# Kernel tuning notes

Measured on AMD Instinct MI355X. Metric: run time of the kernel, lower is better.

The kernel has to match this reference:

```python
import jax, jax.numpy as jnp
import numpy as np

VOCAB, EMBED = 50000, 256
MODULES, HEADS, HID = 2, 4, 64
B, S = 8, 2048
LABELS = 16


def setup_inputs() -> dict:
    key = jax.random.key(0)
    ks = jax.random.split(key, 12)
    seqs = jax.random.randint(ks[0], (B, S), 0, VOCAB)
    emb = jax.random.normal(ks[1], (VOCAB, EMBED), jnp.float32) * 0.02
    Wq = jax.random.normal(ks[2], (MODULES, HEADS, HID, EMBED), jnp.float32) * (1.0 / np.sqrt(EMBED))
    bq = jax.random.normal(ks[3], (MODULES, HEADS, HID), jnp.float32) * 0.01
    Wk = jax.random.normal(ks[4], (MODULES, HEADS, HID, EMBED), jnp.float32) * (1.0 / np.sqrt(EMBED))
    bk = jax.random.normal(ks[5], (MODULES, HEADS, HID), jnp.float32) * 0.01
    Wv = jax.random.normal(ks[6], (MODULES, HEADS, HID, EMBED), jnp.float32) * (1.0 / np.sqrt(EMBED))
    bv = jax.random.normal(ks[7], (MODULES, HEADS, HID), jnp.float32) * 0.01
    Wz = jax.random.normal(ks[8], (MODULES, EMBED, HEADS * HID), jnp.float32) * (1.0 / np.sqrt(HEADS * HID))
    bz = jax.random.normal(ks[9], (MODULES, EMBED), jnp.float32) * 0.01
    Wo = jax.random.normal(ks[10], (LABELS, S * EMBED), jnp.float32) * (1.0 / np.sqrt(S * EMBED))
    bo = jax.random.normal(ks[11], (LABELS,), jnp.float32) * 0.01
    return {"seqs": seqs, "emb": emb, "Wq": Wq, "bq": bq, "Wk": Wk, "bk": bk,
            "Wv": Wv, "bv": bv, "Wz": Wz, "bz": bz, "Wo": Wo, "bo": bo}


def _forward(seqs, emb, Wq, bq, Wk, bk, Wv, bv, Wz, bz, Wo, bo):
    x = emb[seqs]  # [B, S, E]
    scale = jnp.float32(EMBED) ** 0.5
    for m in range(MODULES):
        # per-head projections with relu (dropout=0 / eval mode)
        Q = jax.nn.relu(jnp.einsum('bse,hde->bhsd', x, Wq[m]) + bq[m][None, :, None, :])
        K = jax.nn.relu(jnp.einsum('bse,hde->bhsd', x, Wk[m]) + bk[m][None, :, None, :])
        V = jax.nn.relu(jnp.einsum('bse,hde->bhsd', x, Wv[m]) + bv[m][None, :, None, :])
        QK = jnp.einsum('bhsd,bhtd->bhst', Q, K) / scale  # [B,H,S,S]
        # double softmax: first over the query axis (torch dim=1 of [B,S,S]),
        # then over the key axis (torch dim=2)
        A = jax.nn.softmax(QK, axis=2)
        A = jax.nn.softmax(A, axis=3)
        Z = jnp.einsum('bhst,bhtd->bhsd', A, V)  # [B,H,S,HID]
        Zall = jnp.transpose(Z, (0, 2, 1, 3)).reshape(x.shape[0], S, HEADS * HID)
        ZF = jnp.einsum('bsk,ek->bse', Zall, Wz[m]) + bz[m]
        x = ZF + x  # residual (layer_norm=False)
    Xf = x.reshape(x.shape[0], S * EMBED)
    y = jax.nn.sigmoid(Xf @ Wo.T + bo)
    return y


def reference(seqs, emb, Wq, bq, Wk, bk, Wv, bv, Wz, bz, Wo, bo):
    return _forward(seqs, emb, Wq, bq, Wk, bk, Wv, bv, Wz, bz, Wo, bo)
```

## Files before the change

### kernel.cpp

```cpp
#include <hip/hip_runtime.h>
#include <math.h>

#define Bb 8
#define Ss 2048
#define Ee 256
#define Hh 4
#define Dd 64

typedef unsigned short u16;
typedef unsigned int u32;
typedef __attribute__((ext_vector_type(8))) short bf16x8;
typedef __attribute__((ext_vector_type(4))) float f32x4;

__device__ __forceinline__ u16 f2bf(float f) {
  union { float f; u32 u; } c; c.f = f;
  return (u16)((c.u + 0x7FFFu + ((c.u >> 16) & 1u)) >> 16);
}
__device__ __forceinline__ float bf2f(u16 u) {
  union { u32 u; float f; } c; c.u = ((u32)u) << 16;
  return c.f;
}
__device__ __forceinline__ float bf2fs(short s) { return bf2f((u16)s); }

__global__ __launch_bounds__(256) void k_w2b(const float* __restrict__ src,
                                             u16* __restrict__ dst) {
  int idx = (blockIdx.x * 256 + threadIdx.x) * 4;
  float4 v = *reinterpret_cast<const float4*>(src + idx);
  ushort4 o;
  o.x = f2bf(v.x); o.y = f2bf(v.y); o.z = f2bf(v.z); o.w = f2bf(v.w);
  *reinterpret_cast<ushort4*>(dst + idx) = o;
}

__global__ __launch_bounds__(256) void k_gather(const int* __restrict__ seqs,
                                                const float* __restrict__ emb,
                                                float* __restrict__ x,
                                                u16* __restrict__ xb) {
  int idx = blockIdx.x * 256 + threadIdx.x;
  int row = idx >> 6, c4 = idx & 63;
  int tok = seqs[row];
  float4 v = reinterpret_cast<const float4*>(emb)[(size_t)tok * 64 + c4];
  reinterpret_cast<float4*>(x)[(size_t)row * 64 + c4] = v;
  ushort4 o;
  o.x = f2bf(v.x); o.y = f2bf(v.y); o.z = f2bf(v.z); o.w = f2bf(v.w);
  reinterpret_cast<ushort4*>(xb)[(size_t)row * 64 + c4] = o;
}

__global__ __launch_bounds__(256) void k_qkvm(const u16* __restrict__ xb,
    const u16* __restrict__ Wqb, const u16* __restrict__ Wkb, const u16* __restrict__ Wvb,
    const float* __restrict__ bq, const float* __restrict__ bk, const float* __restrict__ bv,
    u16* __restrict__ Qf, u16* __restrict__ Kf, u16* __restrict__ Vf, int mod) {
  __shared__ short Xs[128][72];
  __shared__ short Ws[128][72];
  int tid = threadIdx.x;
  int bn = blockIdx.x;
  int arr = bn >> 1, coff = (bn & 1) << 7;
  const u16* W = (arr == 0 ? Wqb : arr == 1 ? Wkb : Wvb) + (size_t)mod * 256 * 256;
  const float* bias = (arr == 0 ? bq : arr == 1 ? bk : bv) + mod * 256;
  u16* Out = (arr == 0 ? Qf : arr == 1 ? Kf : Vf);
  int s0 = blockIdx.y * 128;
  int lr = tid >> 1, lc = (tid & 1) << 5;
  int w = tid >> 6, lane = tid & 63, ml = lane & 15, q = lane >> 4;
  int sh = (w >> 1) << 6, th = (w & 1) << 6;
  f32x4 acc[4][4] = {};
  for (int k0 = 0; k0 < 256; k0 += 64) {
#pragma unroll
    for (int hh = 0; hh < 4; hh++) {
      *reinterpret_cast<bf16x8*>(&Xs[lr][lc + hh * 8]) =
          *reinterpret_cast<const bf16x8*>(xb + (size_t)(s0 + lr) * Ee + k0 + lc + hh * 8);
      *reinterpret_cast<bf16x8*>(&Ws[lr][lc + hh * 8]) =
          *reinterpret_cast<const bf16x8*>(W + (size_t)(coff + lr) * Ee + k0 + lc + hh * 8);
    }
    __syncthreads();
#pragma unroll
    for (int ks = 0; ks < 2; ks++) {
      bf16x8 af[4], bfr[4];
#pragma unroll
      for (int mt = 0; mt < 4; mt++)
        af[mt] = *reinterpret_cast<const bf16x8*>(&Xs[sh + mt * 16 + ml][ks * 32 + q * 8]);
#pragma unroll
      for (int nt = 0; nt < 4; nt++)
        bfr[nt] = *reinterpret_cast<const bf16x8*>(&Ws[th + nt * 16 + ml][ks * 32 + q * 8]);
#pragma unroll
      for (int mt = 0; mt < 4; mt++)
#pragma unroll
        for (int nt = 0; nt < 4; nt++)
          acc[mt][nt] = __builtin_amdgcn_mfma_f32_16x16x32_bf16(af[mt], bfr[nt], acc[mt][nt], 0, 0, 0);
    }
    __syncthreads();
  }
#pragma unroll
  for (int mt = 0; mt < 4; mt++)
#pragma unroll
    for (int nt = 0; nt < 4; nt++)
#pragma unroll
      for (int r = 0; r < 4; r++) {
        int gm = s0 + sh + mt * 16 + q * 4 + r;
        int cc = coff + th + nt * 16 + ml;
        float v = acc[mt][nt][r] + bias[cc];
        Out[(size_t)gm * Ee + cc] = f2bf(v > 0.f ? v : 0.f);
      }
}

__global__ __launch_bounds__(256) void k_vt(const u16* __restrict__ Vf,
                                            u16* __restrict__ Vt) {
  __shared__ u16 T[64][72];
  int tid = threadIdx.x;
  int t0 = blockIdx.x * 64;
  int z = blockIdx.y;
  int b = z >> 2, h = z & 3;
  int lr = tid >> 2, lc = (tid & 3) << 4;
#pragma unroll
  for (int hh = 0; hh < 2; hh++) {
    bf16x8 v = *reinterpret_cast<const bf16x8*>(
        Vf + (size_t)(b * Ss + t0 + lr) * Ee + h * Dd + lc + hh * 8);
#pragma unroll
    for (int j = 0; j < 8; j++) T[lr][lc + hh * 8 + j] = (u16)v[j];
  }
  __syncthreads();
#pragma unroll
  for (int j = 0; j < 16; j++) {
    Vt[((size_t)z * Dd + lr) * Ss + t0 + lc + j] = T[lc + j][lr];
  }
}

__global__ __launch_bounds__(256) void k_vsum(const u16* __restrict__ Vt,
                                              float* __restrict__ SV) {
  int z = blockIdx.y;
  int d = blockIdx.x * 4 + (threadIdx.x >> 6);
  int lane = threadIdx.x & 63;
  const u16* row = Vt + ((size_t)z * Dd + d) * Ss;
  float s = 0.f;
#pragma unroll
  for (int it = 0; it < 4; it++) {
    bf16x8 v = *reinterpret_cast<const bf16x8*>(row + it * 512 + lane * 8);
#pragma unroll
    for (int j = 0; j < 8; j++) s += bf2fs(v[j]);
  }
#pragma unroll
  for (int off = 32; off; off >>= 1) s += __shfl_xor(s, off);
  if (lane == 0) SV[(size_t)z * Dd + d] = s;
}

__global__ __launch_bounds__(256) void k_csum(const u16* __restrict__ Qf,
    const u16* __restrict__ Kf, float* __restrict__ icl) {
  __shared__ short Qs[128 * 72];
  __shared__ short Ks[128 * 72];
  __shared__ float csm[4][64];
  int tid = threadIdx.x;
  int z = blockIdx.y, b = z >> 2, h = z & 3;
  const u16* Qb = Qf + (size_t)b * Ss * Ee + h * Dd;
  const u16* Kb = Kf + (size_t)b * Ss * Ee + h * Dd;
  int t0 = blockIdx.x * 128;
  int lr = tid >> 1, lc = (tid & 1) << 5;
#pragma unroll
  for (int hh = 0; hh < 4; hh++)
    *reinterpret_cast<bf16x8*>(&Ks[lr * 72 + lc + hh * 8]) =
        *reinterpret_cast<const bf16x8*>(Kb + (size_t)(t0 + lr) * Ee + lc + hh * 8);
  int w = tid >> 6, lane = tid & 63, ml = lane & 15, q = lane >> 4;
  int sh = (w >> 1) << 6, th = (w & 1) << 6;
  float csum[4] = {};
  for (int s0 = 0; s0 < Ss; s0 += 128) {
    __syncthreads();
#pragma unroll
    for (int hh = 0; hh < 4; hh++)
      *reinterpret_cast<bf16x8*>(&Qs[lr * 72 + lc + hh * 8]) =
          *reinterpret_cast<const bf16x8*>(Qb + (size_t)(s0 + lr) * Ee + lc + hh * 8);
    __syncthreads();
    f32x4 acc[4][4] = {};
#pragma unroll
    for (int ks = 0; ks < 2; ks++) {
      bf16x8 af[4], bf[4];
#pragma unroll
      for (int mt = 0; mt < 4; mt++)
        af[mt] = *reinterpret_cast<const bf16x8*>(&Qs[(sh + mt * 16 + ml) * 72 + ks * 32 + q * 8]);
#pragma unroll
      for (int nt = 0; nt < 4; nt++)
        bf[nt] = *reinterpret_cast<const bf16x8*>(&Ks[(th + nt * 16 + ml) * 72 + ks * 32 + q * 8]);
#pragma unroll
      for (int mt = 0; mt < 4; mt++)
#pragma unroll
        for (int nt = 0; nt < 4; nt++)
          acc[mt][nt] = __builtin_amdgcn_mfma_f32_16x16x32_bf16(af[mt], bf[nt], acc[mt][nt], 0, 0, 0);
    }
#pragma unroll
    for (int nt = 0; nt < 4; nt++)
#pragma unroll
      for (int mt = 0; mt < 4; mt++)
#pragma unroll
        for (int r = 0; r < 4; r++)
          csum[nt] += __expf(acc[mt][nt][r] * 0.0625f);
  }
#pragma unroll
  for (int nt = 0; nt < 4; nt++) {
    csum[nt] += __shfl_xor(csum[nt], 16);
    csum[nt] += __shfl_xor(csum[nt], 32);
  }
  if (lane < 16) {
#pragma unroll
    for (int nt = 0; nt < 4; nt++) csm[w][nt * 16 + ml] = csum[nt];
  }
  __syncthreads();
  if (tid < 128) {
    int half = tid >> 6, c = tid & 63;
    float l = csm[half][c] + csm[half + 2][c];
    icl[(size_t)z * Ss + t0 + half * 64 + c] = 1.f / l;
  }
}

__global__ __launch_bounds__(256) void k_att(const u16* __restrict__ Qf,
    const u16* __restrict__ Kf, const u16* __restrict__ Vt,
    const float* __restrict__ icl, const float* __restrict__ SV,
    u16* __restrict__ Zb) {
  __shared__ short Qs[128 * 72];
  __shared__ short Ks[64 * 72];
  __shared__ short Vs[64 * 72];
  __shared__ short A2s[128 * 76];
  __shared__ float rs_s[2][128];
  int tid = threadIdx.x;
  int z = blockIdx.y, b = z >> 2, h = z & 3;
  const u16* Qb = Qf + (size_t)b * Ss * Ee + h * Dd;
  const u16* Kb = Kf + (size_t)b * Ss * Ee + h * Dd;
  const u16* VtZ = Vt + (size_t)z * Dd * Ss;
  const float* iclz = icl + (size_t)z * Ss;
  int s0 = blockIdx.x * 128;
  int lr = tid >> 1, lc = (tid & 1) << 5;
#pragma unroll
  for (int hh = 0; hh < 4; hh++)
    *reinterpret_cast<bf16x8*>(&Qs[lr * 72 + lc + hh * 8]) =
        *reinterpret_cast<const bf16x8*>(Qb + (size_t)(s0 + lr) * Ee + lc + hh * 8);
  int w = tid >> 6, lane = tid & 63, ml = lane & 15, q = lane >> 4;
  int ws = (w >> 1) << 6, wt = (w & 1) << 5;
  f32x4 acc2[2][4] = {};
  f32x4 rsv[4] = {};
  for (int t0 = 0; t0 < Ss; t0 += 64) {
    __syncthreads();
    if (tid < 128) {
      int r2 = tid >> 1, h2 = (tid & 1) << 5;
#pragma unroll
      for (int j = 0; j < 4; j++)
        *reinterpret_cast<bf16x8*>(&Ks[r2 * 72 + h2 + j * 8]) =
            *reinterpret_cast<const bf16x8*>(Kb + (size_t)(t0 + r2) * Ee + h2 + j * 8);
    } else {
      int t2 = tid - 128;
      int r2 = t2 >> 1, h2 = (t2 & 1) << 5;
#pragma unroll
      for (int j = 0; j < 4; j++)
        *reinterpret_cast<bf16x8*>(&Vs[r2 * 72 + h2 + j * 8]) =
            *reinterpret_cast<const bf16x8*>(VtZ + (size_t)r2 * Ss + t0 + h2 + j * 8);
    }
    __syncthreads();
    f32x4 acc[4][2] = {};
#pragma unroll
    for (int ks = 0; ks < 2; ks++) {
      bf16x8 af[4], bf[2];
#pragma unroll
      for (int mt = 0; mt < 4; mt++)
        af[mt] = *reinterpret_cast<const bf16x8*>(&Qs[(ws + mt * 16 + ml) * 72 + ks * 32 + q * 8]);
#pragma unroll
      for (int nt = 0; nt < 2; nt++)
        bf[nt] = *reinterpret_cast<const bf16x8*>(&Ks[(wt + nt * 16 + ml) * 72 + ks * 32 + q * 8]);
#pragma unroll
      for (int mt = 0; mt < 4; mt++)
#pragma unroll
        for (int nt = 0; nt < 2; nt++)
          acc[mt][nt] = __builtin_amdgcn_mfma_f32_16x16x32_bf16(af[mt], bf[nt], acc[mt][nt], 0, 0, 0);
    }
#pragma unroll
    for (int nt = 0; nt < 2; nt++) {
      float ic = iclz[t0 + wt + nt * 16 + ml];
#pragma unroll
      for (int mt = 0; mt < 4; mt++)
#pragma unroll
        for (int r = 0; r < 4; r++) {
          float e1 = __expf(acc[mt][nt][r] * 0.0625f) * ic;
          float p = e1 * (1.f + e1 * (0.5f + e1 * (0.166666667f +
                    e1 * (0.0416666667f + e1 * 0.00833333333f))));
          rsv[mt][r] += p;
          A2s[(ws + mt * 16 + q * 4 + r) * 76 + wt + nt * 16 + ml] = (short)f2bf(p);
        }
    }
    __syncthreads();
#pragma unroll
    for (int ks = 0; ks < 2; ks++) {
      bf16x8 af2[2], bv[4];
#pragma unroll
      for (int mt2 = 0; mt2 < 2; mt2++)
        af2[mt2] = *reinterpret_cast<const bf16x8*>(&A2s[(w * 32 + mt2 * 16 + ml) * 76 + ks * 32 + q * 8]);
#pragma unroll
      for (int nt = 0; nt < 4; nt++)
        bv[nt] = *reinterpret_cast<const bf16x8*>(&Vs[(nt * 16 + ml) * 72 + ks * 32 + q * 8]);
#pragma unroll
      for (int mt2 = 0; mt2 < 2; mt2++)
#pragma unroll
        for (int nt = 0; nt < 4; nt++)
          acc2[mt2][nt] = __builtin_amdgcn_mfma_f32_16x16x32_bf16(af2[mt2], bv[nt], acc2[mt2][nt], 0, 0, 0);
    }
  }
#pragma unroll
  for (int mt = 0; mt < 4; mt++)
#pragma unroll
    for (int r = 0; r < 4; r++) {
      float v = rsv[mt][r];
      v += __shfl_xor(v, 1); v += __shfl_xor(v, 2);
      v += __shfl_xor(v, 4); v += __shfl_xor(v, 8);
      if (ml == 0) rs_s[w & 1][ws + mt * 16 + q * 4 + r] = v;
    }
  __syncthreads();
  const float* SVz = SV + (size_t)z * Dd;
#pragma unroll
  for (int mt2 = 0; mt2 < 2; mt2++)
#pragma unroll
    for (int r = 0; r < 4; r++) {
      int row = w * 32 + mt2 * 16 + q * 4 + r;
      float inv = 1.f / (2048.f + rs_s[0][row] + rs_s[1][row]);
#pragma unroll
      for (int nt = 0; nt < 4; nt++) {
        float o = (SVz[nt * 16 + ml] + acc2[mt2][nt][r]) * inv;
        Zb[(size_t)(b * Ss + s0 + row) * Ee + h * Dd + nt * 16 + ml] = f2bf(o);
      }
    }
}

__global__ __launch_bounds__(256) void k_zfm(const u16* __restrict__ Zb,
    const u16* __restrict__ Wzb, const float* __restrict__ bzp,
    float* __restrict__ x, u16* __restrict__ xb, int mod) {
  __shared__ short Zs[128][72];
  __shared__ short Ws[128][72];
  int tid = threadIdx.x;
  int coff = blockIdx.x << 7;
  const u16* W = Wzb + (size_t)mod * 256 * 256;
  const float* bias = bzp + mod * Ee;
  int s0 = blockIdx.y * 128;
  int lr = tid >> 1, lc = (tid & 1) << 5;
  int w = tid >> 6, lane = tid & 63, ml = lane & 15, q = lane >> 4;
  int sh = (w >> 1) << 6, th = (w & 1) << 6;
  f32x4 acc[4][4] = {};
  for (int k0 = 0; k0 < 256; k0 += 64) {
#pragma unroll
    for (int hh = 0; hh < 4; hh++) {
      *reinterpret_cast<bf16x8*>(&Zs[lr][lc + hh * 8]) =
          *reinterpret_cast<const bf16x8*>(Zb + (size_t)(s0 + lr) * Ee + k0 + lc + hh * 8);
      *reinterpret_cast<bf16x8*>(&Ws[lr][lc + hh * 8]) =
          *reinterpret_cast<const bf16x8*>(W + (size_t)(coff + lr) * Ee + k0 + lc + hh * 8);
    }
    __syncthreads();
#pragma unroll
    for (int ks = 0; ks < 2; ks++) {
      bf16x8 af[4], bfr[4];
#pragma unroll
      for (int mt = 0; mt < 4; mt++)
        af[mt] = *reinterpret_cast<const bf16x8*>(&Zs[sh + mt * 16 + ml][ks * 32 + q * 8]);
#pragma unroll
      for (int nt = 0; nt < 4; nt++)
        bfr[nt] = *reinterpret_cast<const bf16x8*>(&Ws[th + nt * 16 + ml][ks * 32 + q * 8]);
#pragma unroll
      for (int mt = 0; mt < 4; mt++)
#pragma unroll
        for (int nt = 0; nt < 4; nt++)
          acc[mt][nt] = __builtin_amdgcn_mfma_f32_16x16x32_bf16(af[mt], bfr[nt], acc[mt][nt], 0, 0, 0);
    }
    __syncthreads();
  }
#pragma unroll
  for (int mt = 0; mt < 4; mt++)
#pragma unroll
    for (int nt = 0; nt < 4; nt++)
#pragma unroll
      for (int r = 0; r < 4; r++) {
        int gm = s0 + sh + mt * 16 + q * 4 + r;
        int gn = coff + th + nt * 16 + ml;
        float xv = x[(size_t)gm * Ee + gn] + acc[mt][nt][r] + bias[gn];
        x[(size_t)gm * Ee + gn] = xv;
        xb[(size_t)gm * Ee + gn] = f2bf(xv);
      }
}

__global__ __launch_bounds__(256) void k_final1(const float* __restrict__ x,
    const float* __restrict__ Wo, float* __restrict__ part) {
  int c = blockIdx.x, l = blockIdx.y, b = blockIdx.z;
  int tid = threadIdx.x;
  const float4* xr = reinterpret_cast<const float4*>(x + (size_t)b * (Ss * Ee) + c * 8192);
  const float4* wr = reinterpret_cast<const float4*>(Wo + (size_t)l * (Ss * Ee) + c * 8192);
  float sum = 0.f;
  for (int i = tid; i < 2048; i += 256) {
    float4 a = xr[i], w = wr[i];
    sum += a.x * w.x + a.y * w.y + a.z * w.z + a.w * w.w;
  }
  __shared__ float red[256];
  red[tid] = sum;
  __syncthreads();
  for (int o = 128; o; o >>= 1) {
    if (tid < o) red[tid] += red[tid + o];
    __syncthreads();
  }
  if (tid == 0) part[((b * 16 + l) << 6) + c] = red[0];
}

__global__ void k_final2(const float* __restrict__ part, const float* __restrict__ bo,
                         float* __restrict__ out) {
  int idx = threadIdx.x;
  int b = idx >> 4, l = idx & 15;
  float s = 0.f;
  for (int c = 0; c < 64; c++) s += part[((b * 16 + l) << 6) + c];
  s += bo[l];
  out[idx] = 1.f / (1.f + __expf(-s));
}

extern "C" void kernel_launch(void* const* d_in, const int* in_sizes, int n_in,
                              void* d_out, int out_size, void* d_ws, size_t ws_size,
                              hipStream_t stream) {
  const int*   seqs = (const int*)d_in[0];
  const float* emb  = (const float*)d_in[1];
  const float* Wq   = (const float*)d_in[2];
  const float* bq   = (const float*)d_in[3];
  const float* Wk   = (const float*)d_in[4];
  const float* bk   = (const float*)d_in[5];
  const float* Wv   = (const float*)d_in[6];
  const float* bv   = (const float*)d_in[7];
  const float* Wz   = (const float*)d_in[8];
  const float* bz   = (const float*)d_in[9];
  const float* Wo   = (const float*)d_in[10];
  const float* bo   = (const float*)d_in[11];
  float* out = (float*)d_out;
  float* ws  = (float*)d_ws;

  float* x    = ws;
  u16*   xb   = (u16*)(ws + 4194304);
  u16*   Qf   = (u16*)(ws + 6291456);
  u16*   Kf   = (u16*)(ws + 8388608);
  u16*   Vf   = (u16*)(ws + 10485760);
  u16*   Vt   = (u16*)(ws + 12582912);
  u16*   Zb   = (u16*)(ws + 14680064);
  float* SV   = ws + 16777216;
  float* part = ws + 16779264;
  u16*   Wqb  = (u16*)(ws + 16787456);
  u16*   Wkb  = (u16*)(ws + 16852992);
  u16*   Wvb  = (u16*)(ws + 16918528);
  u16*   Wzb  = (u16*)(ws + 16984064);
  float* icl  = ws + 17049600;

  k_gather<<<(Bb * Ss * 64) / 256, 256, 0, stream>>>(seqs, emb, x, xb);
  k_w2b<<<131072 / 1024, 256, 0, stream>>>(Wq, Wqb);
  k_w2b<<<131072 / 1024, 256, 0, stream>>>(Wk, Wkb);
  k_w2b<<<131072 / 1024, 256, 0, stream>>>(Wv, Wvb);
  k_w2b<<<131072 / 1024, 256, 0, stream>>>(Wz, Wzb);

  for (int m = 0; m < 2; m++) {
    k_qkvm<<<dim3(6, 128), 256, 0, stream>>>(xb, Wqb, Wkb, Wvb, bq, bk, bv, Qf, Kf, Vf, m);
    k_vt<<<dim3(32, 32), 256, 0, stream>>>(Vf, Vt);
    k_vsum<<<dim3(16, 32), 256, 0, stream>>>(Vt, SV);
    k_csum<<<dim3(16, 32), 256, 0, stream>>>(Qf, Kf, icl);
    k_att<<<dim3(16, 32), 256, 0, stream>>>(Qf, Kf, Vt, icl, SV, Zb);
    k_zfm<<<dim3(2, 128), 256, 0, stream>>>(Zb, Wzb, bz, x, xb, m);
  }

  k_final1<<<dim3(64, 16, 8), 256, 0, stream>>>(x, Wo, part);
  k_final2<<<1, 128, 0, stream>>>(part, bo, out);
}
```

Measured before the change: 539.1 us.

## Fold softmax scale into Q, hold K/Q fragments in registers, double-buffer Q tiles

Scales Q by 1/16 when it is stored so the attention kernels skip the per-element multiply. The column-sum kernel now outputs a negative log normalizer, so the attention kernel computes one exp(x+c) instead of an exp followed by a multiply. The K fragments in k_csum and the Q fragments in k_att are loaded once into registers instead of being staged in LDS, and k_csum double-buffers the Q tile to drop a barrier. The exp-series polynomial loses its last term and bf16 rounding is simplified to round-half-up, which changes numerics slightly and raises register pressure.

```diff
diff --git a/kernel.cpp b/kernel.cpp
--- a/kernel.cpp
+++ b/kernel.cpp
@@ -57,6 +57,7 @@
   const u16* W = (arr == 0 ? Wqb : arr == 1 ? Wkb : Wvb) + (size_t)mod * 256 * 256;
   const float* bias = (arr == 0 ? bq : arr == 1 ? bk : bv) + mod * 256;
   u16* Out = (arr == 0 ? Qf : arr == 1 ? Kf : Vf);
+  float oscale = (arr == 0) ? 0.0625f : 1.0f;
   int s0 = blockIdx.y * 128;
   int lr = tid >> 1, lc = (tid & 1) << 5;
   int w = tid >> 6, lane = tid & 63, ml = lane & 15, q = lane >> 4;
@@ -97,7 +98,8 @@
         int gm = s0 + sh + mt * 16 + q * 4 + r;
         int cc = coff + th + nt * 16 + ml;
         float v = acc[mt][nt][r] + bias[cc];
-        Out[(size_t)gm * Ee + cc] = f2bf(v > 0.f ? v : 0.f);
+        v = (v > 0.f ? v : 0.f) * oscale;
+        Out[(size_t)gm * Ee + cc] = f2bf(v);
       }
 }
 
@@ -142,9 +144,8 @@
 }
 
 __global__ __launch_bounds__(256) void k_csum(const u16* __restrict__ Qf,
-    const u16* __restrict__ Kf, float* __restrict__ icl) {
-  __shared__ short Qs[128 * 72];
-  __shared__ short Ks[128 * 72];
+    const u16* __restrict__ Kf, float* __restrict__ llic) {
+  __shared__ short Qs[2][128 * 72];
   __shared__ float csm[4][64];
   int tid = threadIdx.x;
   int z = blockIdx.y, b = z >> 2, h = z & 3;
@@ -152,35 +153,35 @@
   const u16* Kb = Kf + (size_t)b * Ss * Ee + h * Dd;
   int t0 = blockIdx.x * 128;
   int lr = tid >> 1, lc = (tid & 1) << 5;
-#pragma unroll
-  for (int hh = 0; hh < 4; hh++)
-    *reinterpret_cast<bf16x8*>(&Ks[lr * 72 + lc + hh * 8]) =
-        *reinterpret_cast<const bf16x8*>(Kb + (size_t)(t0 + lr) * Ee + lc + hh * 8);
   int w = tid >> 6, lane = tid & 63, ml = lane & 15, q = lane >> 4;
   int sh = (w >> 1) << 6, th = (w & 1) << 6;
+  bf16x8 kb[2][4];
+#pragma unroll
+  for (int ks = 0; ks < 2; ks++)
+#pragma unroll
+    for (int nt = 0; nt < 4; nt++)
+      kb[ks][nt] = *reinterpret_cast<const bf16x8*>(
+          Kb + (size_t)(t0 + th + nt * 16 + ml) * Ee + ks * 32 + q * 8);
   float csum[4] = {};
+  int p = 0;
   for (int s0 = 0; s0 < Ss; s0 += 128) {
-    __syncthreads();
 #pragma unroll
     for (int hh = 0; hh < 4; hh++)
-      *reinterpret_cast<bf16x8*>(&Qs[lr * 72 + lc + hh * 8]) =
+      *reinterpret_cast<bf16x8*>(&Qs[p][lr * 72 + lc + hh * 8]) =
           *reinterpret_cast<const bf16x8*>(Qb + (size_t)(s0 + lr) * Ee + lc + hh * 8);
     __syncthreads();
     f32x4 acc[4][4] = {};
 #pragma unroll
     for (int ks = 0; ks < 2; ks++) {
-      bf16x8 af[4], bf[4];
-#pragma unroll
-      for (int mt = 0; mt < 4; mt++)
-        af[mt] = *reinterpret_cast<const bf16x8*>(&Qs[(sh + mt * 16 + ml) * 72 + ks * 32 + q * 8]);
-#pragma unroll
-      for (int nt = 0; nt < 4; nt++)
-        bf[nt] = *reinterpret_cast<const bf16x8*>(&Ks[(th + nt * 16 + ml) * 72 + ks * 32 + q * 8]);
+      bf16x8 af[4];
+#pragma unroll
+      for (int mt = 0; mt < 4; mt++)
+        af[mt] = *reinterpret_cast<const bf16x8*>(&Qs[p][(sh + mt * 16 + ml) * 72 + ks * 32 + q * 8]);
 #pragma unroll
       for (int mt = 0; mt < 4; mt++)
 #pragma unroll
         for (int nt = 0; nt < 4; nt++)
-          acc[mt][nt] = __builtin_amdgcn_mfma_f32_16x16x32_bf16(af[mt], bf[nt], acc[mt][nt], 0, 0, 0);
+          acc[mt][nt] = __builtin_amdgcn_mfma_f32_16x16x32_bf16(af[mt], kb[ks][nt], acc[mt][nt], 0, 0, 0);
     }
 #pragma unroll
     for (int nt = 0; nt < 4; nt++)
@@ -188,7 +189,8 @@
       for (int mt = 0; mt < 4; mt++)
 #pragma unroll
         for (int r = 0; r < 4; r++)
-          csum[nt] += __expf(acc[mt][nt][r] * 0.0625f);
+          csum[nt] += __expf(acc[mt][nt][r]);
+    p ^= 1;
   }
 #pragma unroll
   for (int nt = 0; nt < 4; nt++) {
@@ -203,15 +205,14 @@
   if (tid < 128) {
     int half = tid >> 6, c = tid & 63;
     float l = csm[half][c] + csm[half + 2][c];
-    icl[(size_t)z * Ss + t0 + half * 64 + c] = 1.f / l;
+    llic[(size_t)z * Ss + t0 + half * 64 + c] = -__logf(l);
   }
 }
 
 __global__ __launch_bounds__(256) void k_att(const u16* __restrict__ Qf,
     const u16* __restrict__ Kf, const u16* __restrict__ Vt,
-    const float* __restrict__ icl, const float* __restrict__ SV,
+    const float* __restrict__ llic, const float* __restrict__ SV,
     u16* __restrict__ Zb) {
-  __shared__ short Qs[128 * 72];
   __shared__ short Ks[64 * 72];
   __shared__ short Vs[64 * 72];
   __shared__ short A2s[128 * 76];
@@ -221,15 +222,17 @@
   const u16* Qb = Qf + (size_t)b * Ss * Ee + h * Dd;
   const u16* Kb = Kf + (size_t)b * Ss * Ee + h * Dd;
   const u16* VtZ = Vt + (size_t)z * Dd * Ss;
-  const float* iclz = icl + (size_t)z * Ss;
+  const float* lz = llic + (size_t)z * Ss;
   int s0 = blockIdx.x * 128;
-  int lr = tid >> 1, lc = (tid & 1) << 5;
-#pragma unroll
-  for (int hh = 0; hh < 4; hh++)
-    *reinterpret_cast<bf16x8*>(&Qs[lr * 72 + lc + hh * 8]) =
-        *reinterpret_cast<const bf16x8*>(Qb + (size_t)(s0 + lr) * Ee + lc + hh * 8);
   int w = tid >> 6, lane = tid & 63, ml = lane & 15, q = lane >> 4;
-  int ws = (w >> 1) << 6, wt = (w & 1) << 5;
+  int wsd = (w >> 1) << 6, wt = (w & 1) << 5;
+  bf16x8 qa[2][4];
+#pragma unroll
+  for (int ks = 0; ks < 2; ks++)
+#pragma unroll
+    for (int mt = 0; mt < 4; mt++)
+      qa[ks][mt] = *reinterpret_cast<const bf16x8*>(
+          Qb + (size_t)(s0 + wsd + mt * 16 + ml) * Ee + ks * 32 + q * 8);
   f32x4 acc2[2][4] = {};
   f32x4 rsv[4] = {};
   for (int t0 = 0; t0 < Ss; t0 += 64) {
@@ -252,10 +255,7 @@
     f32x4 acc[4][2] = {};
 #pragma unroll
     for (int ks = 0; ks < 2; ks++) {
-      bf16x8 af[4], bf[2];
-#pragma unroll
-      for (int mt = 0; mt < 4; mt++)
-        af[mt] = *reinterpret_cast<const bf16x8*>(&Qs[(ws + mt * 16 + ml) * 72 + ks * 32 + q * 8]);
+      bf16x8 bf[2];
 #pragma unroll
       for (int nt = 0; nt < 2; nt++)
         bf[nt] = *reinterpret_cast<const bf16x8*>(&Ks[(wt + nt * 16 + ml) * 72 + ks * 32 + q * 8]);
@@ -263,20 +263,21 @@
       for (int mt = 0; mt < 4; mt++)
 #pragma unroll
         for (int nt = 0; nt < 2; nt++)
-          acc[mt][nt] = __builtin_amdgcn_mfma_f32_16x16x32_bf16(af[mt], bf[nt], acc[mt][nt], 0, 0, 0);
+          acc[mt][nt] = __builtin_amdgcn_mfma_f32_16x16x32_bf16(qa[ks][mt], bf[nt], acc[mt][nt], 0, 0, 0);
     }
 #pragma unroll
     for (int nt = 0; nt < 2; nt++) {
-      float ic = iclz[t0 + wt + nt * 16 + ml];
+      float lcv = lz[t0 + wt + nt * 16 + ml];
 #pragma unroll
       for (int mt = 0; mt < 4; mt++)
 #pragma unroll
         for (int r = 0; r < 4; r++) {
-          float e1 = __expf(acc[mt][nt][r] * 0.0625f) * ic;
-          float p = e1 * (1.f + e1 * (0.5f + e1 * (0.166666667f +
-                    e1 * (0.0416666667f + e1 * 0.00833333333f))));
+          float e1 = __expf(acc[mt][nt][r] + lcv);
+          float p = e1 * (1.f + e1 * (0.5f + e1 * (0.166666667f + e1 * 0.0416666667f)));
           rsv[mt][r] += p;
-          A2s[(ws + mt * 16 + q * 4 + r) * 76 + wt + nt * 16 + ml] = (short)f2bf(p);
+          union { float f; u32 u; } cv; cv.f = p;
+          A2s[(wsd + mt * 16 + q * 4 + r) * 76 + wt + nt * 16 + ml] =
+              (short)((cv.u + 0x8000u) >> 16);
         }
     }
     __syncthreads();
@@ -303,7 +304,7 @@
       float v = rsv[mt][r];
       v += __shfl_xor(v, 1); v += __shfl_xor(v, 2);
       v += __shfl_xor(v, 4); v += __shfl_xor(v, 8);
-      if (ml == 0) rs_s[w & 1][ws + mt * 16 + q * 4 + r] = v;
+      if (ml == 0) rs_s[w & 1][wsd + mt * 16 + q * 4 + r] = v;
     }
   __syncthreads();
   const float* SVz = SV + (size_t)z * Dd;
@@ -437,7 +438,7 @@
   u16*   Wkb  = (u16*)(ws + 16852992);
   u16*   Wvb  = (u16*)(ws + 16918528);
   u16*   Wzb  = (u16*)(ws + 16984064);
-  float* icl  = ws + 17049600;
+  float* llic = ws + 17049600;
 
   k_gather<<<(Bb * Ss * 64) / 256, 256, 0, stream>>>(seqs, emb, x, xb);
   k_w2b<<<131072 / 1024, 256, 0, stream>>>(Wq, Wqb);
@@ -449,8 +450,8 @@
     k_qkvm<<<dim3(6, 128), 256, 0, stream>>>(xb, Wqb, Wkb, Wvb, bq, bk, bv, Qf, Kf, Vf, m);
     k_vt<<<dim3(32, 32), 256, 0, stream>>>(Vf, Vt);
     k_vsum<<<dim3(16, 32), 256, 0, stream>>>(Vt, SV);
-    k_csum<<<dim3(16, 32), 256, 0, stream>>>(Qf, Kf, icl);
-    k_att<<<dim3(16, 32), 256, 0, stream>>>(Qf, Kf, Vt, icl, SV, Zb);
+    k_csum<<<dim3(16, 32), 256, 0, stream>>>(Qf, Kf, llic);
+    k_att<<<dim3(16, 32), 256, 0, stream>>>(Qf, Kf, Vt, llic, SV, Zb);
     k_zfm<<<dim3(2, 128), 256, 0, stream>>>(Zb, Wzb, bz, x, xb, m);
   }
 
```

New measurement: 519.8 us. 3.6% less time.
